# Kernel optimization log

Measured on AMD Instinct MI355X. Metric: run time of the kernel, lower is better.

## Reference

```python
import jax, jax.numpy as jnp
import numpy as np

N = 10000      # nodes
E = 640000     # edges (avg degree 64)
D = 128        # embedding_size
L = 3          # num_layers=4 -> 1 + (4-2) = 3 conv layers


def setup_inputs() -> dict:
    key = jax.random.key(0)
    ks = jax.random.split(key, 4)
    z = jax.random.normal(ks[0], (N, D), dtype=jnp.float32)
    edge_index = jax.random.randint(ks[1], (2, E), 0, N, dtype=jnp.int32)
    # per-layer GCN weights/bias and LayerNorm affine params, stacked over layers
    Ws = jax.random.normal(ks[2], (L, D, D), dtype=jnp.float32) / np.sqrt(D).astype(np.float32)
    bs = jnp.zeros((L, D), dtype=jnp.float32)
    gammas = jnp.ones((L, D), dtype=jnp.float32)
    betas = jnp.zeros((L, D), dtype=jnp.float32)
    return {"z": z, "edge_index": edge_index, "Ws": Ws, "bs": bs,
            "gammas": gammas, "betas": betas}


def _layernorm(x, g, b, eps=1e-5):
    mu = jnp.mean(x, axis=-1, keepdims=True)
    var = jnp.var(x, axis=-1, keepdims=True)
    return (x - mu) * jax.lax.rsqrt(var + eps) * g + b


def reference(z, edge_index, Ws, bs, gammas, betas):
    # GCNConv (PyG default): add self-loops, symmetric normalization
    loops = jnp.arange(N, dtype=edge_index.dtype)
    src = jnp.concatenate([edge_index[0], loops])   # [E+N]
    dst = jnp.concatenate([edge_index[1], loops])   # [E+N]
    deg = jax.ops.segment_sum(jnp.ones(src.shape[0], z.dtype), dst, num_segments=N)
    dinv = jax.lax.rsqrt(jnp.maximum(deg, 1.0))
    norm = dinv[src] * dinv[dst]                    # [E+N]

    x = z
    for i in range(L):
        xw = x @ Ws[i]                              # [N, D] dense transform
        msg = xw[src] * norm[:, None]               # gather + scale  [E+N, D]
        x = jax.ops.segment_sum(msg, dst, num_segments=N) + bs[i]  # scatter-add
        x = _layernorm(x, gammas[i], betas[i])
        x = jax.nn.gelu(x)
        # F.dropout(p=0.1) omitted: deterministic eval-mode reference
    return x
```

## Files before the change

kernel.cpp:

```cpp
#include <hip/hip_runtime.h>

#define DD 128
#define D2 64
#define BW_DST 32
#define BW_SHIFT 5
#define BATCH 4096
#define NBPAD 320
#define P2CAP 6144

struct alignas(8) Rec { unsigned int meta; float w; };

__device__ __forceinline__ unsigned int bf16rne(float f) {
    unsigned int u = __float_as_uint(f);
    unsigned int r = ((u >> 16) & 1u) + 0x7fffu;
    return (u + r) >> 16;
}
__device__ __forceinline__ float bflo(unsigned int v) { return __uint_as_float(v << 16); }
__device__ __forceinline__ float bfhi(unsigned int v) { return __uint_as_float(v & 0xFFFF0000u); }

__global__ void zero_bsum(int* __restrict__ bsum) {
    bsum[threadIdx.x] = 0;
}


__global__ __launch_bounds__(256) void bucket_count(
    const int* __restrict__ dst, int E, int* __restrict__ bsum, int NB)
{
    __shared__ int cnt[NBPAD];
    int t = threadIdx.x;
    for (int b = t; b < NB; b += 256) cnt[b] = 0;
    __syncthreads();
    int gtid = blockIdx.x * 256 + t, gsz = gridDim.x * 256;
    for (int e = gtid; e < E; e += gsz) atomicAdd(&cnt[dst[e] >> BW_SHIFT], 1);
    __syncthreads();
    for (int b = t; b < NB; b += 256) if (cnt[b]) atomicAdd(&bsum[b], cnt[b]);
}

__global__ void scan_bsum(const int* __restrict__ bsum, int* __restrict__ bbase,
                          int* __restrict__ bcur, int* __restrict__ row_ptr,
                          int NB, int N, int E)
{
    __shared__ int part[256];
    int t = threadIdx.x;
    int chunk = (NB + 255) / 256;
    int lo = t * chunk, hi = min(lo + chunk, NB);
    int s = 0;
    for (int b = lo; b < hi; ++b) s += bsum[b];
    part[t] = s;
    __syncthreads();
    for (int o = 1; o < 256; o <<= 1) {
        int v = (t >= o) ? part[t - o] : 0;
        __syncthreads();
        part[t] += v;
        __syncthreads();
    }
    int run = (t == 0) ? 0 : part[t - 1];
    for (int b = lo; b < hi; ++b) {
        bbase[b] = run;
        bcur[b] = run;
        run += bsum[b];
    }
    if (t == 0) row_ptr[N] = E;
}

__global__ __launch_bounds__(256) void bucket_fill(
    const int* __restrict__ src, const int* __restrict__ dst, int E,
    int* __restrict__ bcur, unsigned int* __restrict__ bcsr, int NB)
{
    __shared__ unsigned short sbkt[BATCH];
    __shared__ unsigned short sbkt2[BATCH];
    __shared__ int cnt[NBPAD];
    __shared__ int boff[NBPAD];
    __shared__ int gbase[NBPAD];
    __shared__ int lcur[NBPAD];
    __shared__ unsigned int staged[BATCH];
    int t = threadIdx.x;

    for (int base = blockIdx.x * BATCH; base < E; base += gridDim.x * BATCH) {
        int n = min(E - base, BATCH);
        for (int b = t; b < NBPAD; b += 256) cnt[b] = 0;
        __syncthreads();
        for (int i = t; i < n; i += 256) {
            int d = dst[base + i];
            int bk = d >> BW_SHIFT;
            sbkt[i] = (unsigned short)bk;
            atomicAdd(&cnt[bk], 1);
        }
        __syncthreads();
        if (t < 64) {
            int lo = t * 5;
            int c0 = cnt[lo], c1 = cnt[lo + 1], c2 = cnt[lo + 2],
                c3 = cnt[lo + 3], c4 = cnt[lo + 4];
            int s = c0 + c1 + c2 + c3 + c4;
            int v = s;
            #pragma unroll
            for (int o = 1; o < 64; o <<= 1) { int u = __shfl_up(v, o, 64); if (t >= o) v += u; }
            int e0 = v - s;
            int e1 = e0 + c0, e2 = e1 + c1, e3 = e2 + c2, e4 = e3 + c3;
            boff[lo] = e0; boff[lo + 1] = e1; boff[lo + 2] = e2;
            boff[lo + 3] = e3; boff[lo + 4] = e4;
            lcur[lo] = e0; lcur[lo + 1] = e1; lcur[lo + 2] = e2;
            lcur[lo + 3] = e3; lcur[lo + 4] = e4;
            if (c0) gbase[lo]     = atomicAdd(&bcur[lo],     c0);
            if (c1) gbase[lo + 1] = atomicAdd(&bcur[lo + 1], c1);
            if (c2) gbase[lo + 2] = atomicAdd(&bcur[lo + 2], c2);
            if (c3) gbase[lo + 3] = atomicAdd(&bcur[lo + 3], c3);
            if (c4) gbase[lo + 4] = atomicAdd(&bcur[lo + 4], c4);
        }
        __syncthreads();
        for (int i = t; i < n; i += 256) {
            int e = base + i;
            int ss = src[e], dd = dst[e];
            int bk = sbkt[i];
            int p = atomicAdd(&lcur[bk], 1);
            staged[p] = (unsigned int)ss | ((unsigned int)(dd & (BW_DST - 1)) << 27);
            sbkt2[p] = (unsigned short)bk;
        }
        __syncthreads();
        for (int i = t; i < n; i += 256) {
            int bk = sbkt2[i];
            bcsr[gbase[bk] + (i - boff[bk])] = staged[i];
        }
        __syncthreads();
    }
}

__global__ __launch_bounds__(256) void fine_sort(
    const int* __restrict__ bbase, const unsigned int* __restrict__ bcsr,
    unsigned int* __restrict__ csr4, int* __restrict__ row_ptr,
    float* __restrict__ dinv, int N, int NB, int E)
{
    __shared__ unsigned int staged[P2CAP];
    __shared__ int dcnt[BW_DST];
    __shared__ int dcur[BW_DST];
    int b = blockIdx.x;
    int d0 = b << BW_SHIFT;
    int nd = min(BW_DST, N - d0);
    int base = bbase[b];
    int end  = (b + 1 < NB) ? bbase[b + 1] : E;
    int cnt  = end - base;
    int t = threadIdx.x;
    if (t < BW_DST) dcnt[t] = 0;
    __syncthreads();
    for (int i = t; i < cnt; i += 256) atomicAdd(&dcnt[bcsr[base + i] >> 27], 1);
    __syncthreads();
    if (t < BW_DST) {
        int c = dcnt[t];
        int v = c;
        #pragma unroll
        for (int o = 1; o < BW_DST; o <<= 1) { int u = __shfl_up(v, o, BW_DST); if (t >= o) v += u; }
        int loff = v - c;
        if (t < nd) {
            int node = d0 + t;
            row_ptr[node] = base + loff;
            dinv[node] = rsqrtf((float)(c + 1));
        }
        dcur[t] = loff;
    }
    __syncthreads();
    if (cnt <= P2CAP) {
        for (int i = t; i < cnt; i += 256) {
            unsigned int r = bcsr[base + i];
            int p = atomicAdd(&dcur[r >> 27], 1);
            staged[p] = r;
        }
        __syncthreads();
        for (int i = t; i < cnt; i += 256) csr4[base + i] = staged[i];
    } else {
        for (int i = t; i < cnt; i += 256) {
            unsigned int r = bcsr[base + i];
            int p = atomicAdd(&dcur[r >> 27], 1);
            csr4[base + p] = r;
        }
    }
}

__global__ __launch_bounds__(256) void weight_fill(
    const int* __restrict__ bbase, const unsigned int* __restrict__ csr4,
    const float* __restrict__ dinv, Rec* __restrict__ csr, int NB, int N, int E)
{
    int b = blockIdx.x;
    int base = bbase[b];
    int end  = (b + 1 < NB) ? bbase[b + 1] : E;
    int d0 = b << BW_SHIFT;
    for (int i = base + threadIdx.x; i < end; i += 256) {
        unsigned int r = csr4[i];
        int s = r & 0x07FFFFFFu;
        int d = d0 + (int)(r >> 27);
        Rec rec;
        rec.meta = r;
        rec.w = dinv[s] * dinv[d];
        csr[i] = rec;
    }
}


#define GR 16
__global__ void gemm_xw(const float* __restrict__ x, const float* __restrict__ W,
                        unsigned int* __restrict__ xwb, int N) {
    __shared__ float xs[GR][DD];
    int t = threadIdx.x;
    int r0 = blockIdx.x * GR;
    #pragma unroll
    for (int r = 0; r < GR; ++r) {
        int row = r0 + r;
        xs[r][t] = (row < N) ? x[row * DD + t] : 0.f;
    }
    __syncthreads();
    float acc[GR];
    #pragma unroll
    for (int r = 0; r < GR; ++r) acc[r] = 0.f;
    for (int k = 0; k < DD; k += 4) {
        float w0 = W[(k + 0) * DD + t];
        float w1 = W[(k + 1) * DD + t];
        float w2 = W[(k + 2) * DD + t];
        float w3 = W[(k + 3) * DD + t];
        #pragma unroll
        for (int r = 0; r < GR; ++r) {
            float4 xv = *(const float4*)&xs[r][k];
            acc[r] = fmaf(xv.x, w0, acc[r]);
            acc[r] = fmaf(xv.y, w1, acc[r]);
            acc[r] = fmaf(xv.z, w2, acc[r]);
            acc[r] = fmaf(xv.w, w3, acc[r]);
        }
    }
    #pragma unroll
    for (int r = 0; r < GR; ++r) {
        int row = r0 + r;
        float other = __shfl_xor(acc[r], 1);
        if (row < N && !(t & 1)) {
            unsigned int p = bf16rne(acc[r]) | (bf16rne(other) << 16);
            xwb[row * D2 + (t >> 1)] = p;
        }
    }
}

__global__ __launch_bounds__(512) void agg_gemm(
    const unsigned int* __restrict__ xwb_in, const Rec* __restrict__ csr,
    const int* __restrict__ row_ptr, const float* __restrict__ dinv,
    const float* __restrict__ bias, const float* __restrict__ gamma,
    const float* __restrict__ beta, const float* __restrict__ W,
    unsigned int* __restrict__ xwb_out, int N)
{
    __shared__ float xs[8][DD];
    int t = threadIdx.x;
    int wid = t >> 6, l = t & 63;
    int i = blockIdx.x * 8 + wid;
    if (i < N) {
        int beg = row_ptr[i], end = row_ptr[i + 1];
        float ax = 0.f, ay = 0.f;
        #pragma unroll 8
        for (int j = beg; j < end; ++j) {
            Rec er = csr[j];
            unsigned int v = xwb_in[(er.meta & 0x07FFFFFFu) * D2 + l];
            ax = fmaf(bflo(v), er.w, ax);
            ay = fmaf(bfhi(v), er.w, ay);
        }
        float di = dinv[i], sn = di * di;
        unsigned int v = xwb_in[i * D2 + l];
        ax = fmaf(bflo(v), sn, ax);
        ay = fmaf(bfhi(v), sn, ay);
        float2 b2 = ((const float2*)bias)[l];
        ax += b2.x; ay += b2.y;
        float sum = ax + ay, sq = ax * ax + ay * ay;
        #pragma unroll
        for (int o = 32; o > 0; o >>= 1) { sum += __shfl_xor(sum, o); sq += __shfl_xor(sq, o); }
        float mu   = sum * (1.f / DD);
        float var  = sq * (1.f / DD) - mu * mu;
        float rstd = rsqrtf(var + 1e-5f);
        float2 g2  = ((const float2*)gamma)[l];
        float2 be2 = ((const float2*)beta)[l];
        float y0 = (ax - mu) * rstd * g2.x + be2.x;
        float y1 = (ay - mu) * rstd * g2.y + be2.y;
        y0 = 0.5f * y0 * (1.f + tanhf(0.7978845608f * (y0 + 0.044715f * y0 * y0 * y0)));
        y1 = 0.5f * y1 * (1.f + tanhf(0.7978845608f * (y1 + 0.044715f * y1 * y1 * y1)));
        xs[wid][2 * l]     = y0;
        xs[wid][2 * l + 1] = y1;
    } else {
        xs[wid][2 * l]     = 0.f;
        xs[wid][2 * l + 1] = 0.f;
    }
    __syncthreads();
    int col = t & 127, h = t >> 7;
    float a0 = 0.f, a1 = 0.f;
    for (int k = 0; k < DD; k += 4) {
        float w0 = W[(k + 0) * DD + col];
        float w1 = W[(k + 1) * DD + col];
        float w2 = W[(k + 2) * DD + col];
        float w3 = W[(k + 3) * DD + col];
        float4 x0 = *(const float4*)&xs[h * 2 + 0][k];
        float4 x1 = *(const float4*)&xs[h * 2 + 1][k];
        a0 = fmaf(x0.x, w0, a0); a0 = fmaf(x0.y, w1, a0);
        a0 = fmaf(x0.z, w2, a0); a0 = fmaf(x0.w, w3, a0);
        a1 = fmaf(x1.x, w0, a1); a1 = fmaf(x1.y, w1, a1);
        a1 = fmaf(x1.z, w2, a1); a1 = fmaf(x1.w, w3, a1);
    }
    int row0 = blockIdx.x * 8 + h * 2;
    float o0 = __shfl_xor(a0, 1);
    float o1 = __shfl_xor(a1, 1);
    if (!(t & 1)) {
        if (row0 < N)
            xwb_out[row0 * D2 + (col >> 1)] = bf16rne(a0) | (bf16rne(o0) << 16);
        if (row0 + 1 < N)
            xwb_out[(row0 + 1) * D2 + (col >> 1)] = bf16rne(a1) | (bf16rne(o1) << 16);
    }
}

__global__ __launch_bounds__(256) void agg_ln_gelu(
    const unsigned int* __restrict__ xwb, const Rec* __restrict__ csr,
    const int* __restrict__ row_ptr, const float* __restrict__ dinv,
    const float* __restrict__ bias, const float* __restrict__ gamma,
    const float* __restrict__ beta, float* __restrict__ out, int N)
{
    int i = blockIdx.x * 4 + (threadIdx.x >> 6);
    if (i >= N) return;
    int l = threadIdx.x & 63;
    int beg = row_ptr[i], end = row_ptr[i + 1];
    float ax = 0.f, ay = 0.f;
    #pragma unroll 8
    for (int j = beg; j < end; ++j) {
        Rec er = csr[j];
        unsigned int v = xwb[(er.meta & 0x07FFFFFFu) * D2 + l];
        ax = fmaf(bflo(v), er.w, ax);
        ay = fmaf(bfhi(v), er.w, ay);
    }
    float di = dinv[i], sn = di * di;
    unsigned int v = xwb[i * D2 + l];
    ax = fmaf(bflo(v), sn, ax);
    ay = fmaf(bfhi(v), sn, ay);
    float2 b2 = ((const float2*)bias)[l];
    ax += b2.x; ay += b2.y;
    float sum = ax + ay, sq = ax * ax + ay * ay;
    #pragma unroll
    for (int o = 32; o > 0; o >>= 1) { sum += __shfl_xor(sum, o); sq += __shfl_xor(sq, o); }
    float mu   = sum * (1.f / DD);
    float var  = sq * (1.f / DD) - mu * mu;
    float rstd = rsqrtf(var + 1e-5f);
    float2 g2  = ((const float2*)gamma)[l];
    float2 be2 = ((const float2*)beta)[l];
    float y0 = (ax - mu) * rstd * g2.x + be2.x;
    float y1 = (ay - mu) * rstd * g2.y + be2.y;
    y0 = 0.5f * y0 * (1.f + tanhf(0.7978845608f * (y0 + 0.044715f * y0 * y0 * y0)));
    y1 = 0.5f * y1 * (1.f + tanhf(0.7978845608f * (y1 + 0.044715f * y1 * y1 * y1)));
    float2 o2; o2.x = y0; o2.y = y1;
    ((float2*)out)[i * D2 + l] = o2;
}

static inline size_t align_up(size_t x, size_t a) { return (x + a - 1) & ~(a - 1); }

extern "C" void kernel_launch(void* const* d_in, const int* in_sizes, int n_in,
                              void* d_out, int out_size, void* d_ws, size_t ws_size,
                              hipStream_t stream) {
    const float* z      = (const float*)d_in[0];
    const int*   ei     = (const int*)d_in[1];
    const float* Ws     = (const float*)d_in[2];
    const float* bs     = (const float*)d_in[3];
    const float* gammas = (const float*)d_in[4];
    const float* betas  = (const float*)d_in[5];

    int E  = in_sizes[1] / 2;
    int LD = in_sizes[3];
    int Dd = in_sizes[2] / LD;
    int L  = LD / Dd;
    int N  = in_sizes[0] / Dd;
    int NB = (N + BW_DST - 1) / BW_DST;

    const int* srcp = ei;
    const int* dstp = ei + E;

    char* ws = (char*)d_ws;
    size_t off = 0;
    int* bsum = (int*)(ws + off);        off = align_up(off + (size_t)NBPAD * 4, 256);
    int* bbase = (int*)(ws + off);       off = align_up(off + (size_t)NBPAD * 4, 256);
    int* bcur = (int*)(ws + off);        off = align_up(off + (size_t)NBPAD * 4, 256);
    float* dinv = (float*)(ws + off);    off = align_up(off + (size_t)N * 4, 256);
    int* row_ptr = (int*)(ws + off);     off = align_up(off + (size_t)(N + 1) * 4, 256);
    unsigned int* bcsr = (unsigned int*)(ws + off); off = align_up(off + (size_t)E * 4, 256);
    unsigned int* csr4 = (unsigned int*)(ws + off); off = align_up(off + (size_t)E * 4, 256);
    Rec* csr = (Rec*)(ws + off);         off = align_up(off + (size_t)E * 8, 256);
    unsigned int* xwb_a = (unsigned int*)(ws + off); off = align_up(off + (size_t)N * D2 * 4, 256);
    unsigned int* xwb_b = (unsigned int*)(ws + off); off = align_up(off + (size_t)N * D2 * 4, 256);
    float* dout = (float*)d_out;
    (void)ws_size; (void)n_in; (void)out_size;

    int nb_p1 = (E + BATCH - 1) / BATCH;

    zero_bsum<<<1, NBPAD, 0, stream>>>(bsum);
    bucket_count<<<160, 256, 0, stream>>>(dstp, E, bsum, NB);
    scan_bsum<<<1, 256, 0, stream>>>(bsum, bbase, bcur, row_ptr, NB, N, E);
    bucket_fill<<<nb_p1, 256, 0, stream>>>(srcp, dstp, E, bcur, bcsr, NB);
    fine_sort<<<NB, 256, 0, stream>>>(bbase, bcsr, csr4, row_ptr, dinv, N, NB, E);
    weight_fill<<<NB, 256, 0, stream>>>(bbase, csr4, dinv, csr, NB, N, E);

    gemm_xw<<<(N + GR - 1) / GR, DD, 0, stream>>>(z, Ws, xwb_a, N);

    unsigned int* tin = xwb_a;
    unsigned int* tout = xwb_b;
    for (int li = 0; li < L - 1; ++li) {
        agg_gemm<<<(N + 7) / 8, 512, 0, stream>>>(
            tin, csr, row_ptr, dinv,
            bs + (size_t)li * Dd, gammas + (size_t)li * Dd, betas + (size_t)li * Dd,
            Ws + (size_t)(li + 1) * Dd * Dd, tout, N);
        unsigned int* tmp = tin; tin = tout; tout = tmp;
    }

    agg_ln_gelu<<<(N + 3) / 4, 256, 0, stream>>>(tin, csr, row_ptr, dinv,
                                                 bs + (size_t)(L - 1) * Dd,
                                                 gammas + (size_t)(L - 1) * Dd,
                                                 betas + (size_t)(L - 1) * Dd, dout, N);
}
```

Baseline: 165.5 us.

## Split each node's edge aggregation across two wavefronts with shared-memory reduction

The gather-aggregate loops in agg_gemm and agg_ln_gelu now give each destination node two wavefronts. Each wavefront handles alternate edges, and the two partial sums are combined through shared memory before LayerNorm and GELU. This doubles parallelism and memory-level concurrency for the latency-bound gather, but halves the number of nodes per block. In agg_gemm each block now computes the W product for only 4 rows, so every W element loaded from global/L2 is reused over fewer rows. It also adds a __syncthreads, and half the wavefronts sit idle during the epilogue.

```diff
diff --git a/kernel.cpp b/kernel.cpp
--- a/kernel.cpp
+++ b/kernel.cpp
@@ -242,68 +242,71 @@
     const float* __restrict__ beta, const float* __restrict__ W,
     unsigned int* __restrict__ xwb_out, int N)
 {
-    __shared__ float xs[8][DD];
+    __shared__ float xs[4][DD];
+    __shared__ float2 part[8][64];
     int t = threadIdx.x;
     int wid = t >> 6, l = t & 63;
-    int i = blockIdx.x * 8 + wid;
+    int nd = wid >> 1, member = wid & 1;
+    int i = blockIdx.x * 4 + nd;
+    float ax = 0.f, ay = 0.f;
     if (i < N) {
         int beg = row_ptr[i], end = row_ptr[i + 1];
-        float ax = 0.f, ay = 0.f;
         #pragma unroll 8
-        for (int j = beg; j < end; ++j) {
+        for (int j = beg + member; j < end; j += 2) {
             Rec er = csr[j];
             unsigned int v = xwb_in[(er.meta & 0x07FFFFFFu) * D2 + l];
             ax = fmaf(bflo(v), er.w, ax);
             ay = fmaf(bfhi(v), er.w, ay);
         }
-        float di = dinv[i], sn = di * di;
-        unsigned int v = xwb_in[i * D2 + l];
-        ax = fmaf(bflo(v), sn, ax);
-        ay = fmaf(bfhi(v), sn, ay);
-        float2 b2 = ((const float2*)bias)[l];
-        ax += b2.x; ay += b2.y;
-        float sum = ax + ay, sq = ax * ax + ay * ay;
-        #pragma unroll
-        for (int o = 32; o > 0; o >>= 1) { sum += __shfl_xor(sum, o); sq += __shfl_xor(sq, o); }
-        float mu   = sum * (1.f / DD);
-        float var  = sq * (1.f / DD) - mu * mu;
-        float rstd = rsqrtf(var + 1e-5f);
-        float2 g2  = ((const float2*)gamma)[l];
-        float2 be2 = ((const float2*)beta)[l];
-        float y0 = (ax - mu) * rstd * g2.x + be2.x;
-        float y1 = (ay - mu) * rstd * g2.y + be2.y;
-        y0 = 0.5f * y0 * (1.f + tanhf(0.7978845608f * (y0 + 0.044715f * y0 * y0 * y0)));
-        y1 = 0.5f * y1 * (1.f + tanhf(0.7978845608f * (y1 + 0.044715f * y1 * y1 * y1)));
-        xs[wid][2 * l]     = y0;
-        xs[wid][2 * l + 1] = y1;
-    } else {
-        xs[wid][2 * l]     = 0.f;
-        xs[wid][2 * l + 1] = 0.f;
+    }
+    float2 pp; pp.x = ax; pp.y = ay;
+    part[wid][l] = pp;
+    __syncthreads();
+    if (member == 0) {
+        if (i < N) {
+            float2 p1 = part[wid + 1][l];
+            ax += p1.x; ay += p1.y;
+            float di = dinv[i], sn = di * di;
+            unsigned int v = xwb_in[i * D2 + l];
+            ax = fmaf(bflo(v), sn, ax);
+            ay = fmaf(bfhi(v), sn, ay);
+            float2 b2 = ((const float2*)bias)[l];
+            ax += b2.x; ay += b2.y;
+            float sum = ax + ay, sq = ax * ax + ay * ay;
+            #pragma unroll
+            for (int o = 32; o > 0; o >>= 1) { sum += __shfl_xor(sum, o); sq += __shfl_xor(sq, o); }
+            float mu   = sum * (1.f / DD);
+            float var  = sq * (1.f / DD) - mu * mu;
+            float rstd = rsqrtf(var + 1e-5f);
+            float2 g2  = ((const float2*)gamma)[l];
+            float2 be2 = ((const float2*)beta)[l];
+            float y0 = (ax - mu) * rstd * g2.x + be2.x;
+            float y1 = (ay - mu) * rstd * g2.y + be2.y;
+            y0 = 0.5f * y0 * (1.f + tanhf(0.7978845608f * (y0 + 0.044715f * y0 * y0 * y0)));
+            y1 = 0.5f * y1 * (1.f + tanhf(0.7978845608f * (y1 + 0.044715f * y1 * y1 * y1)));
+            xs[nd][2 * l]     = y0;
+            xs[nd][2 * l + 1] = y1;
+        } else {
+            xs[nd][2 * l]     = 0.f;
+            xs[nd][2 * l + 1] = 0.f;
+        }
     }
     __syncthreads();
     int col = t & 127, h = t >> 7;
-    float a0 = 0.f, a1 = 0.f;
+    float a0 = 0.f;
     for (int k = 0; k < DD; k += 4) {
         float w0 = W[(k + 0) * DD + col];
         float w1 = W[(k + 1) * DD + col];
         float w2 = W[(k + 2) * DD + col];
         float w3 = W[(k + 3) * DD + col];
-        float4 x0 = *(const float4*)&xs[h * 2 + 0][k];
-        float4 x1 = *(const float4*)&xs[h * 2 + 1][k];
+        float4 x0 = *(const float4*)&xs[h][k];
         a0 = fmaf(x0.x, w0, a0); a0 = fmaf(x0.y, w1, a0);
         a0 = fmaf(x0.z, w2, a0); a0 = fmaf(x0.w, w3, a0);
-        a1 = fmaf(x1.x, w0, a1); a1 = fmaf(x1.y, w1, a1);
-        a1 = fmaf(x1.z, w2, a1); a1 = fmaf(x1.w, w3, a1);
-    }
-    int row0 = blockIdx.x * 8 + h * 2;
+    }
+    int row0 = blockIdx.x * 4 + h;
     float o0 = __shfl_xor(a0, 1);
-    float o1 = __shfl_xor(a1, 1);
-    if (!(t & 1)) {
-        if (row0 < N)
-            xwb_out[row0 * D2 + (col >> 1)] = bf16rne(a0) | (bf16rne(o0) << 16);
-        if (row0 + 1 < N)
-            xwb_out[(row0 + 1) * D2 + (col >> 1)] = bf16rne(a1) | (bf16rne(o1) << 16);
-    }
+    if (!(t & 1) && row0 < N)
+        xwb_out[row0 * D2 + (col >> 1)] = bf16rne(a0) | (bf16rne(o0) << 16);
 }
 
 __global__ __launch_bounds__(256) void agg_ln_gelu(
@@ -312,18 +315,28 @@
     const float* __restrict__ bias, const float* __restrict__ gamma,
     const float* __restrict__ beta, float* __restrict__ out, int N)
 {
-    int i = blockIdx.x * 4 + (threadIdx.x >> 6);
-    if (i >= N) return;
-    int l = threadIdx.x & 63;
-    int beg = row_ptr[i], end = row_ptr[i + 1];
+    __shared__ float2 part[4][64];
+    int t = threadIdx.x;
+    int wid = t >> 6, l = t & 63;
+    int nd = wid >> 1, member = wid & 1;
+    int i = blockIdx.x * 2 + nd;
     float ax = 0.f, ay = 0.f;
-    #pragma unroll 8
-    for (int j = beg; j < end; ++j) {
-        Rec er = csr[j];
-        unsigned int v = xwb[(er.meta & 0x07FFFFFFu) * D2 + l];
-        ax = fmaf(bflo(v), er.w, ax);
-        ay = fmaf(bfhi(v), er.w, ay);
-    }
+    if (i < N) {
+        int beg = row_ptr[i], end = row_ptr[i + 1];
+        #pragma unroll 8
+        for (int j = beg + member; j < end; j += 2) {
+            Rec er = csr[j];
+            unsigned int v = xwb[(er.meta & 0x07FFFFFFu) * D2 + l];
+            ax = fmaf(bflo(v), er.w, ax);
+            ay = fmaf(bfhi(v), er.w, ay);
+        }
+    }
+    float2 pp; pp.x = ax; pp.y = ay;
+    part[wid][l] = pp;
+    __syncthreads();
+    if (member != 0 || i >= N) return;
+    float2 p1 = part[wid + 1][l];
+    ax += p1.x; ay += p1.y;
     float di = dinv[i], sn = di * di;
     unsigned int v = xwb[i * D2 + l];
     ax = fmaf(bflo(v), sn, ax);
@@ -397,14 +410,14 @@
     unsigned int* tin = xwb_a;
     unsigned int* tout = xwb_b;
     for (int li = 0; li < L - 1; ++li) {
-        agg_gemm<<<(N + 7) / 8, 512, 0, stream>>>(
+        agg_gemm<<<(N + 3) / 4, 512, 0, stream>>>(
             tin, csr, row_ptr, dinv,
             bs + (size_t)li * Dd, gammas + (size_t)li * Dd, betas + (size_t)li * Dd,
             Ws + (size_t)(li + 1) * Dd * Dd, tout, N);
         unsigned int* tmp = tin; tin = tout; tout = tmp;
     }
 
-    agg_ln_gelu<<<(N + 3) / 4, 256, 0, stream>>>(tin, csr, row_ptr, dinv,
+    agg_ln_gelu<<<(N + 1) / 2, 256, 0, stream>>>(tin, csr, row_ptr, dinv,
                                                  bs + (size_t)(L - 1) * Dd,
                                                  gammas + (size_t)(L - 1) * Dd,
                                                  betas + (size_t)(L - 1) * Dd, dout, N);
```

Measured after the change: 210.3 us. 1.27x slower.

## Unfuse aggregation from dense transform into separate GEMM and aggregate kernels

Applied to the files above, without the earlier changes.

Replaces the fused aggregate+LayerNorm+GELU+next-layer-GEMM kernel with a per-layer pair: a standalone gemm_xw writing bf16 XW, then an aggregation kernel (8 rows per 512-thread block) that writes fp32 activations. The fused kernel read the full weight matrix from global memory for every 8-row block and synchronized on shared memory. The split removes that redundant weight traffic and the barrier, but adds an extra fp32 activation round trip through memory and one more launch per layer.

```diff
diff --git a/kernel.cpp b/kernel.cpp
--- a/kernel.cpp
+++ b/kernel.cpp
@@ -235,97 +235,27 @@
     }
 }
 
-__global__ __launch_bounds__(512) void agg_gemm(
+__global__ __launch_bounds__(512) void agg8(
     const unsigned int* __restrict__ xwb_in, const Rec* __restrict__ csr,
     const int* __restrict__ row_ptr, const float* __restrict__ dinv,
     const float* __restrict__ bias, const float* __restrict__ gamma,
-    const float* __restrict__ beta, const float* __restrict__ W,
-    unsigned int* __restrict__ xwb_out, int N)
-{
-    __shared__ float xs[8][DD];
+    const float* __restrict__ beta, float* __restrict__ out, int N)
+{
     int t = threadIdx.x;
     int wid = t >> 6, l = t & 63;
     int i = blockIdx.x * 8 + wid;
-    if (i < N) {
-        int beg = row_ptr[i], end = row_ptr[i + 1];
-        float ax = 0.f, ay = 0.f;
-        #pragma unroll 8
-        for (int j = beg; j < end; ++j) {
-            Rec er = csr[j];
-            unsigned int v = xwb_in[(er.meta & 0x07FFFFFFu) * D2 + l];
-            ax = fmaf(bflo(v), er.w, ax);
-            ay = fmaf(bfhi(v), er.w, ay);
-        }
-        float di = dinv[i], sn = di * di;
-        unsigned int v = xwb_in[i * D2 + l];
-        ax = fmaf(bflo(v), sn, ax);
-        ay = fmaf(bfhi(v), sn, ay);
-        float2 b2 = ((const float2*)bias)[l];
-        ax += b2.x; ay += b2.y;
-        float sum = ax + ay, sq = ax * ax + ay * ay;
-        #pragma unroll
-        for (int o = 32; o > 0; o >>= 1) { sum += __shfl_xor(sum, o); sq += __shfl_xor(sq, o); }
-        float mu   = sum * (1.f / DD);
-        float var  = sq * (1.f / DD) - mu * mu;
-        float rstd = rsqrtf(var + 1e-5f);
-        float2 g2  = ((const float2*)gamma)[l];
-        float2 be2 = ((const float2*)beta)[l];
-        float y0 = (ax - mu) * rstd * g2.x + be2.x;
-        float y1 = (ay - mu) * rstd * g2.y + be2.y;
-        y0 = 0.5f * y0 * (1.f + tanhf(0.7978845608f * (y0 + 0.044715f * y0 * y0 * y0)));
-        y1 = 0.5f * y1 * (1.f + tanhf(0.7978845608f * (y1 + 0.044715f * y1 * y1 * y1)));
-        xs[wid][2 * l]     = y0;
-        xs[wid][2 * l + 1] = y1;
-    } else {
-        xs[wid][2 * l]     = 0.f;
-        xs[wid][2 * l + 1] = 0.f;
-    }
-    __syncthreads();
-    int col = t & 127, h = t >> 7;
-    float a0 = 0.f, a1 = 0.f;
-    for (int k = 0; k < DD; k += 4) {
-        float w0 = W[(k + 0) * DD + col];
-        float w1 = W[(k + 1) * DD + col];
-        float w2 = W[(k + 2) * DD + col];
-        float w3 = W[(k + 3) * DD + col];
-        float4 x0 = *(const float4*)&xs[h * 2 + 0][k];
-        float4 x1 = *(const float4*)&xs[h * 2 + 1][k];
-        a0 = fmaf(x0.x, w0, a0); a0 = fmaf(x0.y, w1, a0);
-        a0 = fmaf(x0.z, w2, a0); a0 = fmaf(x0.w, w3, a0);
-        a1 = fmaf(x1.x, w0, a1); a1 = fmaf(x1.y, w1, a1);
-        a1 = fmaf(x1.z, w2, a1); a1 = fmaf(x1.w, w3, a1);
-    }
-    int row0 = blockIdx.x * 8 + h * 2;
-    float o0 = __shfl_xor(a0, 1);
-    float o1 = __shfl_xor(a1, 1);
-    if (!(t & 1)) {
-        if (row0 < N)
-            xwb_out[row0 * D2 + (col >> 1)] = bf16rne(a0) | (bf16rne(o0) << 16);
-        if (row0 + 1 < N)
-            xwb_out[(row0 + 1) * D2 + (col >> 1)] = bf16rne(a1) | (bf16rne(o1) << 16);
-    }
-}
-
-__global__ __launch_bounds__(256) void agg_ln_gelu(
-    const unsigned int* __restrict__ xwb, const Rec* __restrict__ csr,
-    const int* __restrict__ row_ptr, const float* __restrict__ dinv,
-    const float* __restrict__ bias, const float* __restrict__ gamma,
-    const float* __restrict__ beta, float* __restrict__ out, int N)
-{
-    int i = blockIdx.x * 4 + (threadIdx.x >> 6);
     if (i >= N) return;
-    int l = threadIdx.x & 63;
     int beg = row_ptr[i], end = row_ptr[i + 1];
     float ax = 0.f, ay = 0.f;
     #pragma unroll 8
     for (int j = beg; j < end; ++j) {
         Rec er = csr[j];
-        unsigned int v = xwb[(er.meta & 0x07FFFFFFu) * D2 + l];
+        unsigned int v = xwb_in[(er.meta & 0x07FFFFFFu) * D2 + l];
         ax = fmaf(bflo(v), er.w, ax);
         ay = fmaf(bfhi(v), er.w, ay);
     }
     float di = dinv[i], sn = di * di;
-    unsigned int v = xwb[i * D2 + l];
+    unsigned int v = xwb_in[i * D2 + l];
     ax = fmaf(bflo(v), sn, ax);
     ay = fmaf(bfhi(v), sn, ay);
     float2 b2 = ((const float2*)bias)[l];
@@ -378,12 +308,13 @@
     unsigned int* bcsr = (unsigned int*)(ws + off); off = align_up(off + (size_t)E * 4, 256);
     unsigned int* csr4 = (unsigned int*)(ws + off); off = align_up(off + (size_t)E * 4, 256);
     Rec* csr = (Rec*)(ws + off);         off = align_up(off + (size_t)E * 8, 256);
-    unsigned int* xwb_a = (unsigned int*)(ws + off); off = align_up(off + (size_t)N * D2 * 4, 256);
-    unsigned int* xwb_b = (unsigned int*)(ws + off); off = align_up(off + (size_t)N * D2 * 4, 256);
+    unsigned int* xwb = (unsigned int*)(ws + off); off = align_up(off + (size_t)N * D2 * 4, 256);
+    float* xb = (float*)(ws + off);      off = align_up(off + (size_t)N * Dd * 4, 256);
     float* dout = (float*)d_out;
     (void)ws_size; (void)n_in; (void)out_size;
 
     int nb_p1 = (E + BATCH - 1) / BATCH;
+    int nb_agg = (N + 7) / 8;
 
     zero_bsum<<<1, NBPAD, 0, stream>>>(bsum);
     bucket_count<<<160, 256, 0, stream>>>(dstp, E, bsum, NB);
@@ -392,20 +323,13 @@
     fine_sort<<<NB, 256, 0, stream>>>(bbase, bcsr, csr4, row_ptr, dinv, N, NB, E);
     weight_fill<<<NB, 256, 0, stream>>>(bbase, csr4, dinv, csr, NB, N, E);
 
-    gemm_xw<<<(N + GR - 1) / GR, DD, 0, stream>>>(z, Ws, xwb_a, N);
-
-    unsigned int* tin = xwb_a;
-    unsigned int* tout = xwb_b;
-    for (int li = 0; li < L - 1; ++li) {
-        agg_gemm<<<(N + 7) / 8, 512, 0, stream>>>(
-            tin, csr, row_ptr, dinv,
-            bs + (size_t)li * Dd, gammas + (size_t)li * Dd, betas + (size_t)li * Dd,
-            Ws + (size_t)(li + 1) * Dd * Dd, tout, N);
-        unsigned int* tmp = tin; tin = tout; tout = tmp;
-    }
-
-    agg_ln_gelu<<<(N + 3) / 4, 256, 0, stream>>>(tin, csr, row_ptr, dinv,
-                                                 bs + (size_t)(L - 1) * Dd,
-                                                 gammas + (size_t)(L - 1) * Dd,
-                                                 betas + (size_t)(L - 1) * Dd, dout, N);
-}
+    const float* cur = z;
+    for (int li = 0; li < L; ++li) {
+        gemm_xw<<<(N + GR - 1) / GR, DD, 0, stream>>>(cur, Ws + (size_t)li * Dd * Dd, xwb, N);
+        float* outp = (li == L - 1) ? dout : xb;
+        agg8<<<nb_agg, 512, 0, stream>>>(xwb, csr, row_ptr, dinv,
+                                         bs + (size_t)li * Dd, gammas + (size_t)li * Dd,
+                                         betas + (size_t)li * Dd, outp, N);
+        cur = outp;
+    }
+}
```

Result: slower. 194.6 us (+17.6%).
